# Kernel optimization log

Hardware: AMD Instinct MI355X
Metric: run time of the kernel (lower is better)

The kernel has to match this reference:

```python
import jax, jax.numpy as jnp
import numpy as np

EPS = 1e-5
NH = 8   # num_heads
P = 8    # patch_size (local window)

def layernorm(x, g, b):
    m = jnp.mean(x, axis=-1, keepdims=True)
    v = jnp.var(x, axis=-1, keepdims=True)
    return (x - m) * jax.lax.rsqrt(v + EPS) * g + b

def axis_embed(pos, nf):
    # DETR-style interleaved sin/cos along one axis -> (L, nf)
    dim_t = 10000.0 ** (2.0 * (jnp.arange(nf) // 2).astype(jnp.float32) / nf)
    p = pos[:, None] / dim_t
    return jnp.stack([jnp.sin(p[:, 0::2]), jnp.cos(p[:, 1::2])], axis=-1).reshape(pos.shape[0], nf)

def pos_embed_2d(E, H, W):
    # (H, W, E): first half of channels encode y, second half encode x
    half = E // 2
    ye = axis_embed(jnp.arange(1, H + 1, dtype=jnp.float32), half)
    xe = axis_embed(jnp.arange(1, W + 1, dtype=jnp.float32), half)
    return jnp.concatenate([jnp.broadcast_to(ye[:, None, :], (H, W, half)),
                            jnp.broadcast_to(xe[None, :, :], (H, W, half))], axis=-1)

def pos_embed_1d(L, E):
    # standard sinusoidal, (L, 1, E)
    pos = jnp.arange(L, dtype=jnp.float32)[:, None]
    div = jnp.exp(jnp.arange(0, E, 2, dtype=jnp.float32) * (-np.log(10000.0) / E))
    pe = jnp.zeros((L, E), jnp.float32)
    pe = pe.at[:, 0::2].set(jnp.sin(pos * div)).at[:, 1::2].set(jnp.cos(pos * div))
    return pe[:, None, :]

def mha(q, k, v, Wq, bq, Wk, bk, Wv, bv, Wo, bo, nh):
    # q,k,v: (B, L, C)
    B, Lq, C = q.shape
    hd = C // nh
    qh = (q @ Wq + bq).reshape(B, Lq, nh, hd)
    kh = (k @ Wk + bk).reshape(B, -1, nh, hd)
    vh = (v @ Wv + bv).reshape(B, -1, nh, hd)
    att = jax.nn.softmax(jnp.einsum('bqhd,bkhd->bhqk', qh, kh) / np.sqrt(hd).astype(np.float32), axis=-1)
    out = jnp.einsum('bhqk,bkhd->bqhd', att, vh).reshape(B, Lq, C)
    return out @ Wo + bo

def win_part(x):
    # (N,T,H,W,C) -> (N*T*nWin, P*P, C)
    N, T, H, W, C = x.shape
    x = x.reshape(N, T, H // P, P, W // P, P, C).transpose(0, 1, 2, 4, 3, 5, 6)
    return x.reshape(-1, P * P, C)

def forward(x, g1, b1, g2, b2, g3, b3, g4, b4,
            sWq, sbq, sWk, sbk, sWv, sbv, sWo, sbo,
            cW1, cb1, dwk, dwb, cW2, cb2,
            tWq, tbq, tWk, tbk, tWv, tbv, tWo, tbo,
            fW1, fb1, fW2, fb2):
    N, T, H, W, C = x.shape
    sl_pos = jnp.tile(pos_embed_2d(C, P, P), (H // P, W // P, 1))  # (H,W,C)
    tem_pos = pos_embed_1d(T, C)                                   # (T,1,C)

    # --- spatial local windowed MHSA (q=k=norm1(x+pos), v=norm1(x)) ---
    qk = win_part(layernorm(x + sl_pos, g1, b1))
    vv = win_part(layernorm(x, g1, b1))
    attn = mha(qk, qk, vv, sWq, sbq, sWk, sbk, sWv, sbv, sWo, sbo, NH)
    attn = attn.reshape(N, T, H // P, W // P, P, P, C).transpose(0, 1, 2, 4, 3, 5, 6).reshape(N, T, H, W, C)
    x = x + attn

    # --- Conv FFN: linear -> depthwise 3x3 -> GELU -> linear ---
    h = layernorm(x, g2, b2) @ cW1 + cb1
    Ch = h.shape[-1]
    h = h.reshape(N * T, H, W, Ch).transpose(0, 3, 1, 2)  # NCHW
    h = jax.lax.conv_general_dilated(h, dwk, (1, 1), 'SAME', feature_group_count=Ch,
                                     dimension_numbers=('NCHW', 'OIHW', 'NCHW')) + dwb[None, :, None, None]
    h = jax.nn.gelu(h, approximate=False)
    h = h.transpose(0, 2, 3, 1).reshape(N, T, H, W, Ch)
    x = x + (h @ cW2 + cb2)

    # --- temporal MHSA over T, tokens are (n,h,w) positions ---
    xt = x.transpose(1, 0, 2, 3, 4).reshape(T, N * H * W, C)
    xt = layernorm(xt, g3, b3)
    qt = layernorm(xt + tem_pos, g3, b3).transpose(1, 0, 2)  # (B,T,C)
    vt = layernorm(xt, g3, b3).transpose(1, 0, 2)
    xt = xt + mha(qt, qt, vt, tWq, tbq, tWk, tbk, tWv, tbv, tWo, tbo, NH).transpose(1, 0, 2)

    # --- FFN; original does x = x + drop3(x) (no residual, doubles output) ---
    xt = layernorm(xt, g4, b4)
    xt = jax.nn.gelu(xt @ fW1 + fb1, approximate=False) @ fW2 + fb2
    xt = xt + xt
    return xt.reshape(T, N, H, W, C).transpose(1, 0, 2, 3, 4)

def setup_inputs() -> dict:
    key = jax.random.key(0)
    N, T, H, W, C, DFF, HID = 4, 16, 32, 32, 256, 1024, 1024
    ks = iter(jax.random.split(key, 64))
    def w(*s):
        return jax.random.normal(next(ks), s, jnp.float32) * 0.02
    inp = dict(x=jax.random.normal(next(ks), (N, T, H, W, C), jnp.float32))
    for i in ('1', '2', '3', '4'):
        inp['g' + i] = jnp.ones((C,), jnp.float32)
        inp['b' + i] = jnp.zeros((C,), jnp.float32)
    for pfx in ('s', 't'):
        inp.update({pfx + 'Wq': w(C, C), pfx + 'bq': jnp.zeros((C,), jnp.float32),
                    pfx + 'Wk': w(C, C), pfx + 'bk': jnp.zeros((C,), jnp.float32),
                    pfx + 'Wv': w(C, C), pfx + 'bv': jnp.zeros((C,), jnp.float32),
                    pfx + 'Wo': w(C, C), pfx + 'bo': jnp.zeros((C,), jnp.float32)})
    inp.update(cW1=w(C, HID), cb1=jnp.zeros((HID,), jnp.float32),
               dwk=w(HID, 1, 3, 3), dwb=jnp.zeros((HID,), jnp.float32),
               cW2=w(HID, C), cb2=jnp.zeros((C,), jnp.float32))
    inp.update(fW1=w(C, DFF), fb1=jnp.zeros((DFF,), jnp.float32),
               fW2=w(DFF, C), fb2=jnp.zeros((C,), jnp.float32))
    return inp

def reference(x, g1, b1, g2, b2, g3, b3, g4, b4,
              sWq, sbq, sWk, sbk, sWv, sbv, sWo, sbo,
              cW1, cb1, dwk, dwb, cW2, cb2,
              tWq, tbq, tWk, tbk, tWv, tbv, tWo, tbo,
              fW1, fb1, fW2, fb2):
    return forward(x, g1, b1, g2, b2, g3, b3, g4, b4,
                   sWq, sbq, sWk, sbk, sWv, sbv, sWo, sbo,
                   cW1, cb1, dwk, dwb, cW2, cb2,
                   tWq, tbq, tWk, tbk, tWv, tbv, tWo, tbo,
                   fW1, fb1, fW2, fb2)
```

## Files before the change

kernel.cpp:

```cpp
#include <hip/hip_runtime.h>
#include <hip/hip_bf16.h>

typedef unsigned short u16;
typedef unsigned int u32;
typedef __attribute__((ext_vector_type(4))) float f32x4;
typedef __attribute__((ext_vector_type(8))) short s16x8;

static constexpr int Nn = 4, Tt = 16, Hh = 32, Ww = 32, Cc = 256;
static constexpr int Ltok = Nn * Tt * Hh * Ww;

__device__ __forceinline__ float bf2f(u16 v) {
  union { u32 u; float f; } t; t.u = ((u32)v) << 16; return t.f;
}
__device__ __forceinline__ u16 f2bf(float f) {
  union { u32 u; float f; } t; t.f = f;
  return (u16)((t.u + 0x7fffu + ((t.u >> 16) & 1u)) >> 16);
}
__device__ __forceinline__ ushort4 pack4(float a, float b, float c, float d) {
  ushort4 r; r.x = f2bf(a); r.y = f2bf(b); r.z = f2bf(c); r.w = f2bf(d); return r;
}
__device__ __forceinline__ float geluf(float x) {
  return 0.5f * x * (1.0f + erff(x * 0.70710678118654752f));
}
__device__ __forceinline__ float wsum(float v) {
#pragma unroll
  for (int o = 32; o > 0; o >>= 1) v += __shfl_xor(v, o, 64);
  return v;
}
__device__ __forceinline__ void ln_stats(float a0, float a1, float a2, float a3,
                                         float& m, float& inv) {
  float s  = wsum(a0 + a1 + a2 + a3);
  float s2 = wsum(a0 * a0 + a1 * a1 + a2 * a2 + a3 * a3);
  m = s * (1.0f / 256.0f);
  float v = s2 * (1.0f / 256.0f) - m * m;
  inv = rsqrtf(v + 1e-5f);
}
__device__ __forceinline__ void gload16(const u16* g, u16* l) {
  __builtin_amdgcn_global_load_lds(
      (const __attribute__((address_space(1))) void*)g,
      (__attribute__((address_space(3))) void*)l, 16, 0, 0);
}

__global__ __launch_bounds__(256) void k_pos(float* __restrict__ pe2d,
                                             float* __restrict__ pe1d,
                                             float* __restrict__ dwkT,
                                             float* __restrict__ zb,
                                             const float* __restrict__ dwk) {
  int idx = blockIdx.x * 256 + threadIdx.x;
  if (idx < 16384) {
    int y = idx >> 11, r = idx & 2047, x = r >> 8, c = r & 255;
    float pos; int cc;
    if (c < 128) { pos = (float)(y + 1); cc = c; }
    else         { pos = (float)(x + 1); cc = c - 128; }
    float e = (float)(cc & ~1) * (1.0f / 128.0f);
    float v = pos / powf(10000.0f, e);
    pe2d[idx] = (cc & 1) ? cosf(v) : sinf(v);
  } else if (idx < 20480) {
    int i = idx - 16384;
    int t = i >> 8, c = i & 255;
    float e = (float)(c & ~1) * (1.0f / 256.0f);
    float v = (float)t * powf(10000.0f, -e);
    pe1d[i] = (c & 1) ? cosf(v) : sinf(v);
  } else if (idx < 29696) {
    int i = idx - 20480;
    int c = i & 1023, tap = i >> 10;
    dwkT[tap * 1024 + c] = dwk[c * 9 + tap];
  } else if (idx < 30720) {
    zb[idx - 29696] = 0.0f;
  }
}

__global__ __launch_bounds__(256) void k_wprep(
    const float* __restrict__ s0, const float* __restrict__ s1,
    const float* __restrict__ s2, const float* __restrict__ s3,
    const float* __restrict__ s4, const float* __restrict__ s5,
    const float* __restrict__ s6, const float* __restrict__ s7,
    const float* __restrict__ cW1, const float* __restrict__ cW2,
    const float* __restrict__ fW1, const float* __restrict__ fW2,
    u16* __restrict__ WT) {
  __shared__ float Ls[32][33];
  int b = blockIdx.x;
  const float* src; u16* dst; int Kd, Nd, tb;
  if (b < 512) {
    int seg = b >> 6; tb = b & 63; Kd = 256; Nd = 256;
    const float* tab[8] = {s0, s1, s2, s3, s4, s5, s6, s7};
    src = tab[seg]; dst = WT + seg * 65536;
  } else if (b < 768)  { tb = b - 512;  Kd = 256;  Nd = 1024; src = cW1; dst = WT + 524288; }
  else if (b < 1024)   { tb = b - 768;  Kd = 1024; Nd = 256;  src = cW2; dst = WT + 786432; }
  else if (b < 1280)   { tb = b - 1024; Kd = 256;  Nd = 1024; src = fW1; dst = WT + 1048576; }
  else                 { tb = b - 1280; Kd = 1024; Nd = 256;  src = fW2; dst = WT + 1310720; }
  int nt = Nd >> 5;
  int tk = tb / nt, tn = tb % nt;
  int r = threadIdx.x >> 3, c0 = (threadIdx.x & 7) * 4;
  float4 v = *(const float4*)&src[(size_t)(tk * 32 + r) * Nd + tn * 32 + c0];
  Ls[r][c0] = v.x; Ls[r][c0 + 1] = v.y; Ls[r][c0 + 2] = v.z; Ls[r][c0 + 3] = v.w;
  __syncthreads();
  *(ushort4*)&dst[(size_t)(tn * 32 + r) * Kd + tk * 32 + c0] =
      pack4(Ls[c0][r], Ls[c0 + 1][r], Ls[c0 + 2][r], Ls[c0 + 3][r]);
}

__global__ __launch_bounds__(256) void k_ln1(const float* __restrict__ x,
                                             const float* __restrict__ g,
                                             const float* __restrict__ b,
                                             const float* __restrict__ pe2d,
                                             u16* __restrict__ qk,
                                             u16* __restrict__ vv) {
  int l = blockIdx.x * 4 + (threadIdx.x >> 6);
  int lane = threadIdx.x & 63, c0 = lane * 4;
  int idx = l & 1023, hh = idx >> 5, ww = idx & 31;
  float4 xv = *(const float4*)&x[(size_t)l * Cc + c0];
  float4 pv = *(const float4*)&pe2d[(((hh & 7) << 3) | (ww & 7)) * Cc + c0];
  float q0 = xv.x + pv.x, q1 = xv.y + pv.y, q2 = xv.z + pv.z, q3 = xv.w + pv.w;
  float mx, ix, mq, iq;
  ln_stats(xv.x, xv.y, xv.z, xv.w, mx, ix);
  ln_stats(q0, q1, q2, q3, mq, iq);
  float4 gv = *(const float4*)&g[c0];
  float4 bv = *(const float4*)&b[c0];
  *(ushort4*)&qk[(size_t)l * Cc + c0] =
      pack4((q0 - mq) * iq * gv.x + bv.x, (q1 - mq) * iq * gv.y + bv.y,
            (q2 - mq) * iq * gv.z + bv.z, (q3 - mq) * iq * gv.w + bv.w);
  *(ushort4*)&vv[(size_t)l * Cc + c0] =
      pack4((xv.x - mx) * ix * gv.x + bv.x, (xv.y - mx) * ix * gv.y + bv.y,
            (xv.z - mx) * ix * gv.z + bv.z, (xv.w - mx) * ix * gv.w + bv.w);
}

__global__ __launch_bounds__(256) void k_lnb(const u16* __restrict__ x,
                                             const float* __restrict__ g,
                                             const float* __restrict__ b,
                                             u16* __restrict__ out) {
  int l = blockIdx.x * 4 + (threadIdx.x >> 6);
  int lane = threadIdx.x & 63, c0 = lane * 4;
  ushort4 xv4 = *(const ushort4*)&x[(size_t)l * Cc + c0];
  float x0 = bf2f(xv4.x), x1 = bf2f(xv4.y), x2 = bf2f(xv4.z), x3 = bf2f(xv4.w);
  float m, inv;
  ln_stats(x0, x1, x2, x3, m, inv);
  float4 gv = *(const float4*)&g[c0];
  float4 bv = *(const float4*)&b[c0];
  *(ushort4*)&out[(size_t)l * Cc + c0] =
      pack4((x0 - m) * inv * gv.x + bv.x, (x1 - m) * inv * gv.y + bv.y,
            (x2 - m) * inv * gv.z + bv.z, (x3 - m) * inv * gv.w + bv.w);
}

__global__ __launch_bounds__(256) void k_ln3b(const u16* __restrict__ xa,
                                              const float* __restrict__ g,
                                              const float* __restrict__ b,
                                              const float* __restrict__ pe1d,
                                              u16* __restrict__ xt_base,
                                              u16* __restrict__ qt,
                                              u16* __restrict__ vt) {
  int l = blockIdx.x * 4 + (threadIdx.x >> 6);
  int lane = threadIdx.x & 63, c0 = lane * 4;
  ushort4 xv4 = *(const ushort4*)&xa[(size_t)l * Cc + c0];
  float x0 = bf2f(xv4.x), x1 = bf2f(xv4.y), x2 = bf2f(xv4.z), x3 = bf2f(xv4.w);
  float4 gv = *(const float4*)&g[c0];
  float4 bv = *(const float4*)&b[c0];
  float m, inv;
  ln_stats(x0, x1, x2, x3, m, inv);
  float t0 = (x0 - m) * inv * gv.x + bv.x;
  float t1 = (x1 - m) * inv * gv.y + bv.y;
  float t2 = (x2 - m) * inv * gv.z + bv.z;
  float t3 = (x3 - m) * inv * gv.w + bv.w;
  *(ushort4*)&xt_base[(size_t)l * Cc + c0] = pack4(t0, t1, t2, t3);
  float m2, inv2;
  ln_stats(t0, t1, t2, t3, m2, inv2);
  *(ushort4*)&vt[(size_t)l * Cc + c0] =
      pack4((t0 - m2) * inv2 * gv.x + bv.x, (t1 - m2) * inv2 * gv.y + bv.y,
            (t2 - m2) * inv2 * gv.z + bv.z, (t3 - m2) * inv2 * gv.w + bv.w);
  int tt = (l >> 10) & 15;
  float4 pv = *(const float4*)&pe1d[tt * Cc + c0];
  float s0 = t0 + pv.x, s1 = t1 + pv.y, s2 = t2 + pv.z, s3 = t3 + pv.w;
  float m3, inv3;
  ln_stats(s0, s1, s2, s3, m3, inv3);
  *(ushort4*)&qt[(size_t)l * Cc + c0] =
      pack4((s0 - m3) * inv3 * gv.x + bv.x, (s1 - m3) * inv3 * gv.y + bv.y,
            (s2 - m3) * inv3 * gv.z + bv.z, (s3 - m3) * inv3 * gv.w + bv.w);
}

template <int MODE>
__global__ __launch_bounds__(256, 2) void k_sgemm(const u16* __restrict__ A,
                                                  const u16* __restrict__ WT,
                                                  const float* __restrict__ bias,
                                                  const void* __restrict__ res,
                                                  void* __restrict__ out,
                                                  int ldout) {
  __shared__ u16 SMEM[32768];
  const int tid = threadIdx.x;
  const int wave = tid >> 6, lane = tid & 63;
  const int fr = lane & 15, fs = lane >> 4;
  const int r0base = blockIdx.x * 128;
  s16x8 wreg[4][8];
#pragma unroll
  for (int ni = 0; ni < 4; ++ni)
#pragma unroll
    for (int kt = 0; kt < 8; ++kt)
      wreg[ni][kt] = *(const s16x8*)&WT[(size_t)(wave * 64 + ni * 16 + fr) * 256 +
                                        kt * 32 + fs * 8];
  auto stage = [&](int buf, int r0) {
    u16* Ad = SMEM + buf * 8192;
#pragma unroll
    for (int i = 0; i < 4; ++i) {
      int idx = i * 256 + tid;
      int row = idx >> 5, s = idx & 31;
      gload16(A + (size_t)(r0 + row) * 256 + ((s ^ row) << 3), &Ad[idx * 8]);
    }
  };
  float* sc = (float*)(SMEM + 16384) + wave * 2048;
  u16* sc2 = SMEM + 16384 + wave * 2048;
  stage(0, r0base);
  __syncthreads();
#pragma unroll 1
  for (int c = 0; c < 4; ++c) {
    if (c < 3) stage((c + 1) & 1, r0base + (c + 1) * 32);
    const u16* As = SMEM + (c & 1) * 8192;
    f32x4 acc[2][4] = {};
#pragma unroll
    for (int kt = 0; kt < 8; ++kt) {
      s16x8 a0 = *(const s16x8*)&As[(fr * 32 + ((kt * 4 + fs) ^ fr)) * 8];
      s16x8 a1 = *(const s16x8*)&As[((16 + fr) * 32 + ((kt * 4 + fs) ^ (16 + fr))) * 8];
#pragma unroll
      for (int ni = 0; ni < 4; ++ni) {
        acc[0][ni] = __builtin_amdgcn_mfma_f32_16x16x32_bf16(a0, wreg[ni][kt],
                                                             acc[0][ni], 0, 0, 0);
        acc[1][ni] = __builtin_amdgcn_mfma_f32_16x16x32_bf16(a1, wreg[ni][kt],
                                                             acc[1][ni], 0, 0, 0);
      }
    }
    const int r0 = r0base + c * 32;
    if constexpr (MODE == 5) {
      u16* o = (u16*)out;
#pragma unroll
      for (int ni = 0; ni < 4; ++ni) {
        float bv = bias[wave * 64 + ni * 16 + fr];
#pragma unroll
        for (int mi = 0; mi < 2; ++mi)
#pragma unroll
          for (int r = 0; r < 4; ++r) {
            int row = mi * 16 + fs * 4 + r;
            int col = ni * 16 + fr;
            sc2[col * 32 + row] = f2bf(acc[mi][ni][r] + bv);
          }
      }
#pragma unroll
      for (int p = 0; p < 4; ++p) {
        int gcl = p * 16 + (lane >> 2);
        int sub = lane & 3;
        uint4 u = *(const uint4*)&sc2[gcl * 32 + sub * 8];
        int gc = wave * 64 + gcl;
        *(uint4*)&o[(size_t)gc * (size_t)Ltok + r0 + sub * 8] = u;
      }
    } else {
#pragma unroll
      for (int mi = 0; mi < 2; ++mi)
#pragma unroll
        for (int ni = 0; ni < 4; ++ni)
#pragma unroll
          for (int r = 0; r < 4; ++r) {
            int row = mi * 16 + fs * 4 + r;
            int col = ni * 16 + fr;
            sc[row * 64 + (col ^ ((row & 7) << 3))] = acc[mi][ni][r];
          }
#pragma unroll
      for (int p = 0; p < 8; ++p) {
        int row = p * 4 + (lane >> 4);
        int c4 = (lane & 15) * 4;
        f32x4 v4 = *(const f32x4*)&sc[row * 64 + (c4 ^ ((row & 7) << 3))];
        int gr = r0 + row;
        int gc = wave * 64 + c4;
        float4 bv4 = *(const float4*)&bias[gc];
        float v[4] = {v4[0] + bv4.x, v4[1] + bv4.y, v4[2] + bv4.z, v4[3] + bv4.w};
        size_t o = (size_t)gr * (size_t)ldout + gc;
        if constexpr (MODE == 1) {
#pragma unroll
          for (int j = 0; j < 4; ++j) v[j] = geluf(v[j]);
        }
        if constexpr (MODE == 3) {
          ushort4 r4 = *(const ushort4*)&((const u16*)res)[(size_t)gr * 256 + gc];
          v[0] += bf2f(r4.x); v[1] += bf2f(r4.y); v[2] += bf2f(r4.z); v[3] += bf2f(r4.w);
        }
        if constexpr (MODE == 7) {
          float4 r4 = *(const float4*)&((const float*)res)[(size_t)gr * 256 + gc];
          v[0] += r4.x; v[1] += r4.y; v[2] += r4.z; v[3] += r4.w;
        }
        *(ushort4*)&((u16*)out)[o] = pack4(v[0], v[1], v[2], v[3]);
      }
    }
    __syncthreads();
  }
}

template <int MODE>
__global__ __launch_bounds__(256, 2) void k_m2(const u16* __restrict__ A,
                                               const u16* __restrict__ BT, int ldbt,
                                               const float* __restrict__ bias,
                                               const void* __restrict__ res,
                                               void* __restrict__ out, int K) {
  __shared__ u16 SMEM[16384];
  const int tid = threadIdx.x;
  const int wave = tid >> 6, lane = tid & 63;
  const int fr = lane & 15, fs = lane >> 4;
  const int bid = blockIdx.x;
  const int m0 = (bid >> 1) * 128, n0 = (bid & 1) * 128;
  const int wm = wave >> 1, wn = wave & 1;
  f32x4 acc[4][4] = {};

  auto stage = [&](int buf, int k0) {
    u16* Ad = SMEM + buf * 8192;
    u16* Bd = Ad + 4096;
#pragma unroll
    for (int i = 0; i < 2; ++i) {
      int idx = i * 256 + tid;
      int row = idx >> 2, s = idx & 3;
      gload16(A + (size_t)(m0 + row) * K + k0 + ((s ^ (row & 3)) << 3), &Ad[idx * 8]);
      gload16(BT + (size_t)(n0 + row) * ldbt + k0 + ((s ^ (row & 3)) << 3),
              &Bd[idx * 8]);
    }
  };
  auto compute = [&](int buf) {
    const u16* As = SMEM + buf * 8192;
    const u16* Bs = As + 4096;
    s16x8 af[4], bfr[4];
#pragma unroll
    for (int i = 0; i < 4; ++i) {
      int ra = wm * 64 + i * 16 + fr;
      af[i] = *(const s16x8*)&As[ra * 32 + ((fs ^ (ra & 3)) << 3)];
      int rb = wn * 64 + i * 16 + fr;
      bfr[i] = *(const s16x8*)&Bs[rb * 32 + ((fs ^ (rb & 3)) << 3)];
    }
#pragma unroll
    for (int mi = 0; mi < 4; ++mi)
#pragma unroll
      for (int ni = 0; ni < 4; ++ni)
        acc[mi][ni] = __builtin_amdgcn_mfma_f32_16x16x32_bf16(af[mi], bfr[ni],
                                                              acc[mi][ni], 0, 0, 0);
  };

  stage(0, 0);
  __syncthreads();
  const int nt = K >> 5;
  int cur = 0;
  for (int t = 0; t < nt; ++t) {
    if (t < nt - 1) stage(cur ^ 1, (t + 1) << 5);
    compute(cur);
    __syncthreads();
    cur ^= 1;
  }
  float* Wl = (float*)SMEM + wave * 2048;
#pragma unroll
  for (int nh = 0; nh < 2; ++nh) {
#pragma unroll
    for (int mi = 0; mi < 4; ++mi)
#pragma unroll
      for (int nq = 0; nq < 2; ++nq) {
        int ni = nh * 2 + nq;
#pragma unroll
        for (int r = 0; r < 4; ++r) {
          int row = mi * 16 + fs * 4 + r;
          int col = nq * 16 + fr;
          Wl[row * 32 + (col ^ ((row & 7) << 2))] = acc[mi][ni][r];
        }
      }
#pragma unroll
    for (int p = 0; p < 8; ++p) {
      int row = p * 8 + (lane >> 3);
      int c4 = (lane & 7) * 4;
      f32x4 v4 = *(const f32x4*)&Wl[row * 32 + (c4 ^ ((row & 7) << 2))];
      int gr = m0 + wm * 64 + row;
      int gc = n0 + wn * 64 + nh * 32 + c4;
      float4 bv4 = *(const float4*)&bias[gc];
      float v[4] = {v4[0] + bv4.x, v4[1] + bv4.y, v4[2] + bv4.z, v4[3] + bv4.w};
      size_t o = (size_t)gr * 256 + gc;
      if constexpr (MODE == 3) {
        ushort4 r4 = *(const ushort4*)&((const u16*)res)[o];
        v[0] += bf2f(r4.x); v[1] += bf2f(r4.y); v[2] += bf2f(r4.z); v[3] += bf2f(r4.w);
        *(ushort4*)&((u16*)out)[o] = pack4(v[0], v[1], v[2], v[3]);
      } else {
        *(float4*)&((float*)out)[o] =
            make_float4(v[0] * 2.0f, v[1] * 2.0f, v[2] * 2.0f, v[3] * 2.0f);
      }
    }
    __syncthreads();
  }
}

__global__ __launch_bounds__(256) void k_sattn2(const u16* __restrict__ Q,
                                                const u16* __restrict__ Kb,
                                                const u16* __restrict__ VT,
                                                u16* __restrict__ ctx) {
  __shared__ u16 P_lds[4][4096];
  const int tid = threadIdx.x;
  const int wave = tid >> 6, lane = tid & 63;
  const int fr = lane & 15, fs = lane >> 4;
  const int wi = blockIdx.x >> 1;
  const int head = (blockIdx.x & 1) * 4 + wave;
  const int ft = wi >> 4, wy = (wi >> 2) & 3, wx = wi & 3;
  const int base = ft * 1024 + wy * 256 + wx * 8;
  const float scale = 0.17677669529663688f;
  const int ch = head * 32 + fs * 8;
  s16x8 ka[4], qb[4];
#pragma unroll
  for (int t4 = 0; t4 < 4; ++t4) {
    int tok = base + (2 * t4 + (fr >> 3)) * 32 + (fr & 7);
    ka[t4] = *(const s16x8*)&Kb[(size_t)tok * 256 + ch];
    qb[t4] = *(const s16x8*)&Q[(size_t)tok * 256 + ch];
  }
  f32x4 s[4][4] = {};
#pragma unroll
  for (int kt = 0; kt < 4; ++kt)
#pragma unroll
    for (int qt = 0; qt < 4; ++qt)
      s[kt][qt] = __builtin_amdgcn_mfma_f32_16x16x32_bf16(ka[kt], qb[qt], s[kt][qt], 0, 0, 0);
  u16* pw = P_lds[wave];
#pragma unroll
  for (int qt = 0; qt < 4; ++qt) {
    float m = -1e30f;
#pragma unroll
    for (int kt = 0; kt < 4; ++kt)
#pragma unroll
      for (int r = 0; r < 4; ++r) m = fmaxf(m, s[kt][qt][r]);
    m = fmaxf(m, __shfl_xor(m, 16, 64));
    m = fmaxf(m, __shfl_xor(m, 32, 64));
    m *= scale;
    float e[4][4];
    float sum = 0.f;
#pragma unroll
    for (int kt = 0; kt < 4; ++kt)
#pragma unroll
      for (int r = 0; r < 4; ++r) {
        e[kt][r] = __expf(s[kt][qt][r] * scale - m);
        sum += e[kt][r];
      }
    sum += __shfl_xor(sum, 16, 64);
    sum += __shfl_xor(sum, 32, 64);
    float il = 1.0f / sum;
    int q = qt * 16 + fr;
    int rowb = q * 128, sw = (q & 7) << 4;
#pragma unroll
    for (int kt = 0; kt < 4; ++kt)
      *(ushort4*)((char*)pw + ((rowb + kt * 32 + fs * 8) ^ sw)) =
          pack4(e[kt][0] * il, e[kt][1] * il, e[kt][2] * il, e[kt][3] * il);
  }
  f32x4 o[4][2] = {};
#pragma unroll
  for (int ks = 0; ks < 2; ++ks) {
    s16x8 vb[2];
#pragma unroll
    for (int nt = 0; nt < 2; ++nt) {
      int d = head * 32 + nt * 16 + fr;
      int tok = base + (ks * 4 + fs) * 32;
      vb[nt] = *(const s16x8*)&VT[(size_t)d * (size_t)Ltok + tok];
    }
#pragma unroll
    for (int qt = 0; qt < 4; ++qt) {
      int q = qt * 16 + fr;
      s16x8 pa = *(const s16x8*)((char*)pw +
                                 ((q * 128 + ks * 64 + fs * 16) ^ ((q & 7) << 4)));
#pragma unroll
      for (int nt = 0; nt < 2; ++nt)
        o[qt][nt] = __builtin_amdgcn_mfma_f32_16x16x32_bf16(pa, vb[nt], o[qt][nt], 0, 0, 0);
    }
  }
#pragma unroll
  for (int qt = 0; qt < 4; ++qt)
#pragma unroll
    for (int r = 0; r < 4; ++r) {
      int q = qt * 16 + fs * 4 + r;
      int tok = base + (q >> 3) * 32 + (q & 7);
#pragma unroll
      for (int nt = 0; nt < 2; ++nt)
        ctx[(size_t)tok * 256 + head * 32 + nt * 16 + fr] = f2bf(o[qt][nt][r]);
    }
}

__global__ __launch_bounds__(256) void k_tattn2(const u16* __restrict__ Q,
                                                const u16* __restrict__ Kb,
                                                const u16* __restrict__ V,
                                                u16* __restrict__ ctx) {
  __shared__ u16 Vs[16 * 256];
  const int tid = threadIdx.x;
  const int b = blockIdx.x;
  const int n = b >> 10, hw = b & 1023;
  const int tok0 = n * 16384 + hw;
#pragma unroll
  for (int i = 0; i < 2; ++i) {
    int chunk = tid * 2 + i;
    int row = chunk >> 5, c8 = (chunk & 31) * 8;
    *(uint4*)&Vs[row * 256 + c8] =
        *(const uint4*)&V[(size_t)(tok0 + row * 1024) * 256 + c8];
  }
  __syncthreads();
  const int wave = tid >> 6, lane = tid & 63;
  const int fr = lane & 15, fs = lane >> 4;
  const float scale = 0.17677669529663688f;
#pragma unroll
  for (int hg = 0; hg < 2; ++hg) {
    int head = wave + hg * 4;
    int ch = head * 32 + fs * 8;
    size_t go = (size_t)(tok0 + fr * 1024) * 256 + ch;
    s16x8 ka = *(const s16x8*)&Kb[go];
    s16x8 qb = *(const s16x8*)&Q[go];
    f32x4 s = {0.f, 0.f, 0.f, 0.f};
    s = __builtin_amdgcn_mfma_f32_16x16x32_bf16(ka, qb, s, 0, 0, 0);
    float m = fmaxf(fmaxf(s[0], s[1]), fmaxf(s[2], s[3]));
    m = fmaxf(m, __shfl_xor(m, 16, 64));
    m = fmaxf(m, __shfl_xor(m, 32, 64));
    m *= scale;
    float e0 = __expf(s[0] * scale - m), e1 = __expf(s[1] * scale - m);
    float e2 = __expf(s[2] * scale - m), e3 = __expf(s[3] * scale - m);
    float sum = e0 + e1 + e2 + e3;
    sum += __shfl_xor(sum, 16, 64);
    sum += __shfl_xor(sum, 32, 64);
    float il = 1.0f / sum;
    e0 *= il; e1 *= il; e2 *= il; e3 *= il;
    float o[8] = {};
#pragma unroll
    for (int kb = 0; kb < 4; ++kb) {
      int src = kb * 16 + fr;
      float p0 = __shfl(e0, src, 64);
      float p1 = __shfl(e1, src, 64);
      float p2 = __shfl(e2, src, 64);
      float p3 = __shfl(e3, src, 64);
#pragma unroll
      for (int r = 0; r < 4; ++r) {
        float p = r == 0 ? p0 : (r == 1 ? p1 : (r == 2 ? p2 : p3));
        uint4 vv = *(const uint4*)&Vs[(kb * 4 + r) * 256 + ch];
        const u16* vp = (const u16*)&vv;
#pragma unroll
        for (int u = 0; u < 8; ++u) o[u] = fmaf(p, bf2f(vp[u]), o[u]);
      }
    }
    size_t co = (size_t)(tok0 + fr * 1024) * 256 + ch;
    *(ushort4*)&ctx[co] = pack4(o[0], o[1], o[2], o[3]);
    *(ushort4*)&ctx[co + 4] = pack4(o[4], o[5], o[6], o[7]);
  }
}

__global__ __launch_bounds__(256) void k_dwconv(const u16* __restrict__ Hin,
                                                const float* __restrict__ dwkT,
                                                const float* __restrict__ dwb,
                                                int ch0, int oco,
                                                u16* __restrict__ Hout) {
  int flat = blockIdx.x * 256 + threadIdx.x;
  int l = flat >> 5, cg = flat & 31, c0 = cg * 8, tc0 = ch0 + c0;
  int frame = l >> 10, idx = l & 1023, hh = idx >> 5, ww = idx & 31;
  float acc[8];
  *(float4*)&acc[0] = *(const float4*)&dwb[tc0];
  *(float4*)&acc[4] = *(const float4*)&dwb[tc0 + 4];
#pragma unroll
  for (int ky = -1; ky <= 1; ++ky) {
    int h2 = hh + ky;
    if (h2 < 0 || h2 >= 32) continue;
#pragma unroll
    for (int kx = -1; kx <= 1; ++kx) {
      int w2 = ww + kx;
      if (w2 < 0 || w2 >= 32) continue;
      int ln = frame * 1024 + h2 * 32 + w2;
      uint4 hv = *(const uint4*)&Hin[(size_t)ln * 256 + c0];
      const u16* hp = (const u16*)&hv;
      int tap = (ky + 1) * 3 + (kx + 1);
      float wk[8];
      *(float4*)&wk[0] = *(const float4*)&dwkT[tap * 1024 + tc0];
      *(float4*)&wk[4] = *(const float4*)&dwkT[tap * 1024 + tc0 + 4];
#pragma unroll
      for (int u = 0; u < 8; ++u) acc[u] = fmaf(bf2f(hp[u]), wk[u], acc[u]);
    }
  }
  size_t ob = (size_t)l * 512 + oco + c0;
  *(ushort4*)&Hout[ob] = pack4(geluf(acc[0]), geluf(acc[1]), geluf(acc[2]), geluf(acc[3]));
  *(ushort4*)&Hout[ob + 4] = pack4(geluf(acc[4]), geluf(acc[5]), geluf(acc[6]), geluf(acc[7]));
}

extern "C" void kernel_launch(void* const* d_in, const int* in_sizes, int n_in,
                              void* d_out, int out_size, void* d_ws, size_t ws_size,
                              hipStream_t stream) {
  (void)in_sizes; (void)n_in; (void)out_size; (void)ws_size;
  const float* x   = (const float*)d_in[0];
  const float* g1  = (const float*)d_in[1];  const float* b1  = (const float*)d_in[2];
  const float* g2  = (const float*)d_in[3];  const float* b2  = (const float*)d_in[4];
  const float* g3  = (const float*)d_in[5];  const float* b3  = (const float*)d_in[6];
  const float* g4  = (const float*)d_in[7];  const float* b4  = (const float*)d_in[8];
  const float* sWq = (const float*)d_in[9];  const float* sbq = (const float*)d_in[10];
  const float* sWk = (const float*)d_in[11]; const float* sbk = (const float*)d_in[12];
  const float* sWv = (const float*)d_in[13]; const float* sbv = (const float*)d_in[14];
  const float* sWo = (const float*)d_in[15]; const float* sbo = (const float*)d_in[16];
  const float* tWq = (const float*)d_in[17]; const float* tbq = (const float*)d_in[18];
  const float* tWk = (const float*)d_in[19]; const float* tbk = (const float*)d_in[20];
  const float* tWv = (const float*)d_in[21]; const float* tbv = (const float*)d_in[22];
  const float* tWo = (const float*)d_in[23]; const float* tbo = (const float*)d_in[24];
  const float* cW1 = (const float*)d_in[25]; const float* cb1 = (const float*)d_in[26];
  const float* dwk = (const float*)d_in[27]; const float* dwb = (const float*)d_in[28];
  const float* cW2 = (const float*)d_in[29]; const float* cb2 = (const float*)d_in[30];
  const float* fW1 = (const float*)d_in[31]; const float* fb1 = (const float*)d_in[32];
  const float* fW2 = (const float*)d_in[33]; const float* fb2 = (const float*)d_in[34];

  char* ws = (char*)d_ws;
  const size_t MB = 1ull << 20;
  float* PE2D = (float*)(ws);
  float* PE1D = (float*)(ws + (64 << 10));
  float* DWKT = (float*)(ws + (80 << 10));
  float* ZB   = (float*)(ws + (116 << 10));
  u16*   WT   = (u16*)(ws + (128 << 10));
  u16* XA  = (u16*)(ws + 4 * MB);
  u16* X1  = (u16*)(ws + 4 * MB);
  u16* B1  = (u16*)(ws + 68 * MB);
  u16* B2  = (u16*)(ws + 100 * MB);
  u16* B3  = (u16*)(ws + 132 * MB);
  u16* B4  = (u16*)(ws + 164 * MB);
  u16* F1  = (u16*)(ws + 4 * MB);
  u16* H1q = B2;
  u16* H2h = B3;

  u16* sWqT = WT;               u16* sWkT = WT + 65536;
  u16* sWvT = WT + 2 * 65536;   u16* sWoT = WT + 3 * 65536;
  u16* tWqT = WT + 4 * 65536;   u16* tWkT = WT + 5 * 65536;
  u16* tWvT = WT + 6 * 65536;   u16* tWoT = WT + 7 * 65536;
  u16* cW1T = WT + 524288;      u16* cW2T = WT + 786432;
  u16* fW1T = WT + 1048576;     u16* fW2T = WT + 1310720;

  dim3 blk(256);
  dim3 gLN(Ltok / 4);
  dim3 gS(512);
  dim3 gM2(1024);

  k_pos<<<dim3(120), blk, 0, stream>>>(PE2D, PE1D, DWKT, ZB, dwk);
  k_wprep<<<dim3(1536), blk, 0, stream>>>(sWq, sWk, sWv, sWo, tWq, tWk, tWv, tWo,
                                          cW1, cW2, fW1, fW2, WT);
  k_ln1<<<gLN, blk, 0, stream>>>(x, g1, b1, PE2D, B1, B2);
  k_sgemm<5><<<gS, blk, 0, stream>>>(B2, sWvT, sbv, nullptr, B3, 0);
  k_sgemm<0><<<gS, blk, 0, stream>>>(B1, sWqT, sbq, nullptr, B2, 256);
  k_sgemm<0><<<gS, blk, 0, stream>>>(B1, sWkT, sbk, nullptr, B4, 256);
  k_sattn2<<<dim3(2048), blk, 0, stream>>>(B2, B4, B3, B1);
  k_sgemm<7><<<gS, blk, 0, stream>>>(B1, sWoT, sbo, x, XA, 256);
  k_lnb<<<gLN, blk, 0, stream>>>(XA, g2, b2, B1);
  for (int h = 0; h < 2; ++h) {
    for (int qq = 0; qq < 2; ++qq) {
      int q = h * 2 + qq;
      k_sgemm<0><<<gS, blk, 0, stream>>>(B1, cW1T + q * 65536, cb1 + q * 256,
                                         nullptr, H1q, 256);
      k_dwconv<<<dim3(Ltok * 32 / 256), blk, 0, stream>>>(H1q, DWKT, dwb,
                                                          q * 256, qq * 256, H2h);
    }
    k_m2<3><<<gM2, blk, 0, stream>>>(H2h, cW2T + h * 512, 1024,
                                     h ? cb2 : ZB, XA, XA, 512);
  }
  k_ln3b<<<gLN, blk, 0, stream>>>(XA, g3, b3, PE1D, B1, B2, B3);
  k_sgemm<0><<<gS, blk, 0, stream>>>(B3, tWvT, tbv, nullptr, B4, 256);
  k_sgemm<0><<<gS, blk, 0, stream>>>(B2, tWqT, tbq, nullptr, X1, 256);
  k_sgemm<0><<<gS, blk, 0, stream>>>(B2, tWkT, tbk, nullptr, B3, 256);
  k_tattn2<<<dim3(4096), blk, 0, stream>>>(X1, B3, B4, B2);
  k_sgemm<3><<<gS, blk, 0, stream>>>(B2, tWoT, tbo, B1, B3, 256);
  k_lnb<<<gLN, blk, 0, stream>>>(B3, g4, b4, B4);
  for (int q = 0; q < 4; ++q)
    k_sgemm<1><<<gS, blk, 0, stream>>>(B4, fW1T + q * 65536, fb1 + q * 256,
                                       nullptr, F1 + q * 256, 1024);
  k_m2<4><<<gM2, blk, 0, stream>>>(F1, fW2T, 1024, fb2, nullptr,
                                   (float*)d_out, 1024);
}
```

Before: 766.7 us.

## Fuse FFN up-projection, GELU and down-projection into one kernel

Replaces the four FFN1 GEMM launches and the separate FFN2 GEMM with a single kernel. Each block keeps a 64-row input tile in LDS, computes 64-column hidden chunks with GELU in registers and LDS, and accumulates the down-projection directly. This removes the write and re-read of the 1024-wide hidden activation through global memory and cuts launches. In exchange, weights are read straight from global memory for every block, and only 1024 blocks of 64 rows run, with syncs inside the hidden loop, which may cap occupancy and MFMA throughput. The k_m2 MODE 4 branch is also removed, so that kernel now always does the residual path.

```diff
diff --git a/kernel.cpp b/kernel.cpp
--- a/kernel.cpp
+++ b/kernel.cpp
@@ -369,16 +369,110 @@
       float4 bv4 = *(const float4*)&bias[gc];
       float v[4] = {v4[0] + bv4.x, v4[1] + bv4.y, v4[2] + bv4.z, v4[3] + bv4.w};
       size_t o = (size_t)gr * 256 + gc;
-      if constexpr (MODE == 3) {
-        ushort4 r4 = *(const ushort4*)&((const u16*)res)[o];
-        v[0] += bf2f(r4.x); v[1] += bf2f(r4.y); v[2] += bf2f(r4.z); v[3] += bf2f(r4.w);
-        *(ushort4*)&((u16*)out)[o] = pack4(v[0], v[1], v[2], v[3]);
-      } else {
-        *(float4*)&((float*)out)[o] =
-            make_float4(v[0] * 2.0f, v[1] * 2.0f, v[2] * 2.0f, v[3] * 2.0f);
-      }
+      ushort4 r4 = *(const ushort4*)&((const u16*)res)[o];
+      v[0] += bf2f(r4.x); v[1] += bf2f(r4.y); v[2] += bf2f(r4.z); v[3] += bf2f(r4.w);
+      *(ushort4*)&((u16*)out)[o] = pack4(v[0], v[1], v[2], v[3]);
     }
     __syncthreads();
+  }
+}
+
+__global__ __launch_bounds__(256, 2) void k_ffn(const u16* __restrict__ A,
+                                                const u16* __restrict__ W1T,
+                                                const float* __restrict__ fb1,
+                                                const u16* __restrict__ W2T,
+                                                const float* __restrict__ fb2,
+                                                float* __restrict__ out) {
+  __shared__ u16 SMEM[20480];
+  const int tid = threadIdx.x;
+  const int wave = tid >> 6, lane = tid & 63;
+  const int fr = lane & 15, fs = lane >> 4;
+  const int r0 = blockIdx.x * 64;
+  u16* Ald = SMEM;
+  u16* Hld = SMEM + 16384;
+#pragma unroll
+  for (int i = 0; i < 8; ++i) {
+    int idx = i * 256 + tid;
+    int row = idx >> 5, s = idx & 31;
+    gload16(A + (size_t)(r0 + row) * 256 + ((s ^ (row & 7)) << 3), &Ald[idx * 8]);
+  }
+  __syncthreads();
+  f32x4 acc[4][4] = {};
+#pragma unroll 1
+  for (int j = 0; j < 16; ++j) {
+    const int hcol = j * 64 + wave * 16 + fr;
+    s16x8 w1f[8];
+#pragma unroll
+    for (int kt = 0; kt < 8; ++kt)
+      w1f[kt] = *(const s16x8*)&W1T[(size_t)hcol * 256 + kt * 32 + fs * 8];
+    f32x4 h[4] = {};
+#pragma unroll
+    for (int kt = 0; kt < 8; ++kt)
+#pragma unroll
+      for (int mi = 0; mi < 4; ++mi) {
+        int row = mi * 16 + fr;
+        s16x8 a = *(const s16x8*)&Ald[row * 256 + (((kt * 4 + fs) ^ (row & 7)) << 3)];
+        h[mi] = __builtin_amdgcn_mfma_f32_16x16x32_bf16(a, w1f[kt], h[mi], 0, 0, 0);
+      }
+    float b1v = fb1[hcol];
+    __syncthreads();
+#pragma unroll
+    for (int mi = 0; mi < 4; ++mi)
+#pragma unroll
+      for (int r = 0; r < 4; ++r) {
+        int row = mi * 16 + fs * 4 + r;
+        int g = (wave * 2 + (fr >> 3)) ^ (row & 7);
+        Hld[row * 64 + g * 8 + (fr & 7)] = f2bf(geluf(h[mi][r] + b1v));
+      }
+    __syncthreads();
+#pragma unroll
+    for (int kk = 0; kk < 2; ++kk) {
+      s16x8 w2f[4];
+#pragma unroll
+      for (int nj = 0; nj < 4; ++nj)
+        w2f[nj] = *(const s16x8*)&W2T[(size_t)(wave * 64 + nj * 16 + fr) * 1024 +
+                                      j * 64 + kk * 32 + fs * 8];
+      s16x8 ha[4];
+#pragma unroll
+      for (int mi = 0; mi < 4; ++mi) {
+        int row = mi * 16 + fr;
+        ha[mi] = *(const s16x8*)&Hld[row * 64 + (((kk * 4 + fs) ^ (row & 7)) << 3)];
+      }
+#pragma unroll
+      for (int mi = 0; mi < 4; ++mi)
+#pragma unroll
+        for (int nj = 0; nj < 4; ++nj)
+          acc[mi][nj] = __builtin_amdgcn_mfma_f32_16x16x32_bf16(ha[mi], w2f[nj],
+                                                                acc[mi][nj], 0, 0, 0);
+    }
+  }
+  float* Wl = (float*)Ald + wave * 2048;
+#pragma unroll
+  for (int nh = 0; nh < 2; ++nh) {
+#pragma unroll
+    for (int mi = 0; mi < 4; ++mi)
+#pragma unroll
+      for (int nq = 0; nq < 2; ++nq) {
+        int ni = nh * 2 + nq;
+#pragma unroll
+        for (int r = 0; r < 4; ++r) {
+          int row = mi * 16 + fs * 4 + r;
+          int col = nq * 16 + fr;
+          Wl[row * 32 + (col ^ ((row & 7) << 2))] = acc[mi][ni][r];
+        }
+      }
+#pragma unroll
+    for (int p = 0; p < 8; ++p) {
+      int row = p * 8 + (lane >> 3);
+      int c4 = (lane & 7) * 4;
+      f32x4 v4 = *(const f32x4*)&Wl[row * 32 + (c4 ^ ((row & 7) << 2))];
+      int gr = r0 + row;
+      int gc = wave * 64 + nh * 32 + c4;
+      float4 bv4 = *(const float4*)&fb2[gc];
+      *(float4*)&out[(size_t)gr * 256 + gc] =
+          make_float4((v4[0] + bv4.x) * 2.0f, (v4[1] + bv4.y) * 2.0f,
+                      (v4[2] + bv4.z) * 2.0f, (v4[3] + bv4.w) * 2.0f);
+    }
   }
 }
 
@@ -605,7 +699,6 @@
   u16* B2  = (u16*)(ws + 100 * MB);
   u16* B3  = (u16*)(ws + 132 * MB);
   u16* B4  = (u16*)(ws + 164 * MB);
-  u16* F1  = (u16*)(ws + 4 * MB);
   u16* H1q = B2;
   u16* H2h = B3;
 
@@ -649,9 +742,5 @@
   k_tattn2<<<dim3(4096), blk, 0, stream>>>(X1, B3, B4, B2);
   k_sgemm<3><<<gS, blk, 0, stream>>>(B2, tWoT, tbo, B1, B3, 256);
   k_lnb<<<gLN, blk, 0, stream>>>(B3, g4, b4, B4);
-  for (int q = 0; q < 4; ++q)
-    k_sgemm<1><<<gS, blk, 0, stream>>>(B4, fW1T + q * 65536, fb1 + q * 256,
-                                       nullptr, F1 + q * 256, 1024);
-  k_m2<4><<<gM2, blk, 0, stream>>>(F1, fW2T, 1024, fb2, nullptr,
-                                   (float*)d_out, 1024);
-}
+  k_ffn<<<dim3(1024), blk, 0, stream>>>(B4, fW1T, fb1, fW2T, fb2, (float*)d_out);
+}
```

Result: no change. 767.2 us (+0.1%).
